# Kernel tuning notes

Hardware: AMD Instinct MI355X
Metric: run time of the kernel (lower is better)

The kernel has to match this reference:

```python
import jax, jax.numpy as jnp
import numpy as np


def setup_inputs() -> dict:
    key = jax.random.key(0)
    ks = jax.random.split(key, 5)
    B, C, H, W = 8, 64, 64, 64
    Ci = 32  # inter_channels = in_channels // 2
    s = 1.0 / np.sqrt(C)
    return {
        "x": jax.random.normal(ks[0], (B, C, H, W), jnp.float32),
        "Wg": jax.random.normal(ks[1], (Ci, C), jnp.float32) * s,
        "bg": jnp.zeros((Ci,), jnp.float32),
        "Wt": jax.random.normal(ks[2], (Ci, C), jnp.float32) * s,
        "bt": jnp.zeros((Ci,), jnp.float32),
        "Wp": jax.random.normal(ks[3], (Ci, C), jnp.float32) * s,
        "bp": jnp.zeros((Ci,), jnp.float32),
        "Ww": jax.random.normal(ks[4], (C, Ci), jnp.float32) * (1.0 / np.sqrt(Ci)),
        "bw": jnp.zeros((C,), jnp.float32),
    }


def _proj(x, Wc, bc):
    # 1x1 conv: (B,C,H,W) -> (B,O,H,W), then flatten spatial -> (B,O,N)
    b, c, h, w = x.shape
    y = jnp.einsum("oc,bchw->bohw", Wc, x) + bc[None, :, None, None]
    return y.reshape(b, Wc.shape[0], h * w)


def reference(x, Wg, bg, Wt, bt, Wp, bp, Ww, bw):
    b, c, h, w = x.shape
    g_x = _proj(x, Wg, bg).transpose(0, 2, 1)      # (B, N, Ci)
    theta_x = _proj(x, Wt, bt).transpose(0, 2, 1)  # (B, N, Ci)
    phi_x = _proj(x, Wp, bp)                        # (B, Ci, N)
    f = jnp.einsum("bnd,bdm->bnm", theta_x, phi_x)  # (B, N, N)
    f_div_C = jax.nn.softmax(f, axis=-1)
    y = jnp.einsum("bnm,bmd->bnd", f_div_C, g_x)    # (B, N, Ci)
    y = y.transpose(0, 2, 1).reshape(b, Wg.shape[0], h, w)
    W_y = jnp.einsum("od,bdhw->bohw", Ww, y) + bw[None, :, None, None]
    return W_y + x
```

## Files before the change

kernel.cpp:

```cpp
#include <hip/hip_runtime.h>
#include <hip/hip_bf16.h>
#include <cstdint>
#include <cstddef>

#define B_ 8
#define C_ 64
#define CI 32
#define N_ 4096

typedef __attribute__((ext_vector_type(8))) short bf16x8;
typedef __attribute__((ext_vector_type(4))) float f32x4;

__device__ __forceinline__ ushort f2bf(float x) {
  union { float f; uint32_t u; } v; v.f = x;
  uint32_t r = v.u + 0x7FFFu + ((v.u >> 16) & 1u);
  return (ushort)(r >> 16);
}

__device__ __forceinline__ uint32_t cvt_pk_bf16(float lo, float hi) {
  uint32_t r;
  asm("v_cvt_pk_bf16_f32 %0, %1, %2" : "=v"(r) : "v"(lo), "v"(hi));
  return r;
}

__global__ __launch_bounds__(256) void proj_kernel(
    const float* __restrict__ x,
    const float* __restrict__ Wg, const float* __restrict__ bg,
    const float* __restrict__ Wt, const float* __restrict__ bt,
    const float* __restrict__ Wp, const float* __restrict__ bp,
    ushort* __restrict__ theta_t, ushort* __restrict__ phi_t,
    ushort* __restrict__ gmat)
{
  const int z = blockIdx.z;
  const float* W; const float* bias;
  if (z == 0)      { W = Wt; bias = bt; }
  else if (z == 1) { W = Wp; bias = bp; }
  else             { W = Wg; bias = bg; }

  const int b = blockIdx.y;
  const int n = blockIdx.x * 256 + threadIdx.x;
  const float* xb = x + ((size_t)b * C_) * N_ + n;

  float acc[CI];
  #pragma unroll
  for (int d = 0; d < CI; ++d) acc[d] = bias[d];

  #pragma unroll
  for (int cc = 0; cc < C_; cc += 8) {
    float xv[8];
    #pragma unroll
    for (int j = 0; j < 8; ++j) xv[j] = xb[(size_t)(cc + j) * N_];
    #pragma unroll
    for (int j = 0; j < 8; ++j)
      #pragma unroll
      for (int d = 0; d < CI; ++d)
        acc[d] = fmaf(W[d * C_ + cc + j], xv[j], acc[d]);
  }

  if (z == 2) {
    #pragma unroll
    for (int d = 0; d < CI; ++d)
      gmat[((size_t)(b * CI) + d) * N_ + n] = f2bf(acc[d]);
  } else {
    const float scale = (z == 0) ? 1.44269504088896340736f : 1.0f;
    uint32_t w[CI / 2];
    #pragma unroll
    for (int k = 0; k < CI / 2; ++k)
      w[k] = (uint32_t)f2bf(acc[2 * k] * scale) |
             ((uint32_t)f2bf(acc[2 * k + 1] * scale) << 16);
    ushort* base = (z == 0) ? theta_t : phi_t;
    uint4* dst = (uint4*)(base + ((size_t)(b * N_) + n) * CI);
    #pragma unroll
    for (int k = 0; k < CI / 8; ++k)
      dst[k] = make_uint4(w[4 * k], w[4 * k + 1], w[4 * k + 2], w[4 * k + 3]);
  }
}

__global__ __launch_bounds__(512, 4) void attn_kernel(
    const ushort* __restrict__ theta_t,
    const ushort* __restrict__ phi_t,
    const ushort* __restrict__ gmat,
    float* __restrict__ yT)
{
  __shared__ ushort Kt[2][64 * 32];
  __shared__ ushort Vt[2][32 * 64];
  __shared__ ushort Pt[8][16 * 64];
  __shared__ float scratch[4][64][12];

  const int tid = threadIdx.x;
  const int lane = tid & 63;
  const int wave = tid >> 6;
  const int qg = wave & 3;
  const int mh = wave >> 2;
  const int bid = blockIdx.x;
  const int b = bid & 7;
  const int n0 = (bid >> 3) * 64;
  const int nw = n0 + qg * 16;
  const int g4 = lane >> 4;
  const int c16 = lane & 15;
  const int sw = (c16 & 7) << 4;

  const bf16x8 qfrag =
      *(const bf16x8*)(theta_t + ((size_t)(b * N_ + nw + c16)) * CI + g4 * 8);

  bf16x8 onesA;
  {
    const short ov = (c16 == 0) ? (short)0x3F80 : (short)0;
    #pragma unroll
    for (int j = 0; j < 8; ++j) onesA[j] = ov;
  }

  f32x4 acc0 = {0.f, 0.f, 0.f, 0.f};
  f32x4 acc1 = {0.f, 0.f, 0.f, 0.f};
  f32x4 acc2 = {0.f, 0.f, 0.f, 0.f};
  float m_run = -INFINITY;

  const char* kf_base = (const char*)Kt[mh] + ((c16 * 64 + g4 * 16) ^ sw);
  char* pw[4];
  #pragma unroll
  for (int mt = 0; mt < 4; ++mt)
    pw[mt] = (char*)Pt[wave] + ((c16 * 128 + mt * 32 + g4 * 8) ^ sw);
  const char* pr[2]; const char* vr[2];
  #pragma unroll
  for (int ks = 0; ks < 2; ++ks) {
    pr[ks] = (const char*)Pt[wave] + ((c16 * 128 + ks * 64 + g4 * 16) ^ sw);
    vr[ks] = (const char*)Vt[mh] + ((c16 * 128 + ks * 64 + g4 * 16) ^ sw);
  }

  const int khalf = tid >> 8;
  const int krem = tid & 255;
  const int km = krem >> 2, kpart = krem & 3;
  const int vd = krem >> 3, vp8 = krem & 7;
  const ushort* kp = phi_t + ((size_t)(b * N_ + khalf * 2048 + km)) * CI + kpart * 8;
  const ushort* vsp = gmat + ((size_t)(b * CI + vd)) * N_ + khalf * 2048 + vp8 * 8;
  char* kdst = (char*)Kt[khalf] + ((km * 64 + kpart * 16) ^ ((km & 7) << 4));
  char* vdst = (char*)Vt[khalf] + ((vd * 128 + vp8 * 16) ^ ((vd & 7) << 4));

  uint4 kreg = *(const uint4*)kp;  kp += 64 * CI;
  uint4 vreg = *(const uint4*)vsp; vsp += 64;
  *(uint4*)kdst = kreg;
  *(uint4*)vdst = vreg;
  __syncthreads();

  const int NT = 2048 / 64;
  for (int t = 0; t < NT; ++t) {
    const bool more = (t + 1 < NT);
    if (more) {
      kreg = *(const uint4*)kp;  kp += 64 * CI;
      vreg = *(const uint4*)vsp; vsp += 64;
    }

    f32x4 f[4];
    __builtin_amdgcn_s_setprio(1);
    #pragma unroll
    for (int mt = 0; mt < 4; ++mt) {
      const bf16x8 kf = *(const bf16x8*)(kf_base + mt * 1024);
      f[mt] = __builtin_amdgcn_mfma_f32_16x16x32_bf16(
          kf, qfrag, (f32x4){0.f, 0.f, 0.f, 0.f}, 0, 0, 0);
    }
    __builtin_amdgcn_s_setprio(0);

    float pm = fmaxf(
        fmaxf(fmaxf(fmaxf(f[0][0], f[0][1]), fmaxf(f[0][2], f[0][3])),
              fmaxf(fmaxf(f[1][0], f[1][1]), fmaxf(f[1][2], f[1][3]))),
        fmaxf(fmaxf(fmaxf(f[2][0], f[2][1]), fmaxf(f[2][2], f[2][3])),
              fmaxf(fmaxf(f[3][0], f[3][1]), fmaxf(f[3][2], f[3][3]))));
    pm = fmaxf(pm, __shfl_xor(pm, 16));
    pm = fmaxf(pm, __shfl_xor(pm, 32));

    if (__any(pm > m_run + 8.f)) {
      const float mnew = fmaxf(m_run, pm);
      const float sc = __builtin_amdgcn_exp2f(m_run - mnew);
      m_run = mnew;
      acc0 *= sc; acc1 *= sc; acc2 *= sc;
    }

    #pragma unroll
    for (int mt = 0; mt < 4; ++mt) {
      const float p0 = __builtin_amdgcn_exp2f(f[mt][0] - m_run);
      const float p1 = __builtin_amdgcn_exp2f(f[mt][1] - m_run);
      const float p2 = __builtin_amdgcn_exp2f(f[mt][2] - m_run);
      const float p3 = __builtin_amdgcn_exp2f(f[mt][3] - m_run);
      uint2 wv;
      wv.x = cvt_pk_bf16(p0, p1);
      wv.y = cvt_pk_bf16(p2, p3);
      *(uint2*)pw[mt] = wv;
    }
    asm volatile("s_waitcnt lgkmcnt(0)" ::: "memory");

    __builtin_amdgcn_s_setprio(1);
    #pragma unroll
    for (int ks = 0; ks < 2; ++ks) {
      const bf16x8 pfrag = *(const bf16x8*)pr[ks];
      const bf16x8 vf0 = *(const bf16x8*)vr[ks];
      const bf16x8 vf1 = *(const bf16x8*)(vr[ks] + 2048);
      acc0 = __builtin_amdgcn_mfma_f32_16x16x32_bf16(vf0, pfrag, acc0, 0, 0, 0);
      acc1 = __builtin_amdgcn_mfma_f32_16x16x32_bf16(vf1, pfrag, acc1, 0, 0, 0);
      acc2 = __builtin_amdgcn_mfma_f32_16x16x32_bf16(onesA, pfrag, acc2, 0, 0, 0);
    }
    __builtin_amdgcn_s_setprio(0);

    __syncthreads();
    if (more) { *(uint4*)kdst = kreg; *(uint4*)vdst = vreg; }
    __syncthreads();
  }

  const float l_own = __shfl(acc2[0], c16, 64);

  if (mh == 1) {
    float* s = scratch[qg][lane];
    s[0] = m_run; s[1] = l_own;
    #pragma unroll
    for (int r = 0; r < 4; ++r) { s[2 + r] = acc0[r]; s[6 + r] = acc1[r]; }
  }
  __syncthreads();
  if (mh == 0) {
    const float* s = scratch[qg][lane];
    const float mb = s[0], lb = s[1];
    const float mM = fmaxf(m_run, mb);
    const float ea = __builtin_amdgcn_exp2f(m_run - mM);
    const float eb = __builtin_amdgcn_exp2f(mb - mM);
    const float inv = 1.0f / (l_own * ea + lb * eb);
    const float fa = ea * inv, fb = eb * inv;
    #pragma unroll
    for (int r = 0; r < 4; ++r) {
      yT[((size_t)(b * CI + g4 * 4 + r)) * N_ + nw + c16] =
          acc0[r] * fa + s[2 + r] * fb;
      yT[((size_t)(b * CI + 16 + g4 * 4 + r)) * N_ + nw + c16] =
          acc1[r] * fa + s[6 + r] * fb;
    }
  }
}

__global__ __launch_bounds__(256) void outproj_kernel(
    const float* __restrict__ yT, const float* __restrict__ Ww,
    const float* __restrict__ bw, const float* __restrict__ x,
    float* __restrict__ out)
{
  const int b = blockIdx.y;
  const int c0 = blockIdx.z * 16;
  const int n = blockIdx.x * 256 + threadIdx.x;
  float acc[16];
  #pragma unroll
  for (int i = 0; i < 16; ++i) acc[i] = bw[c0 + i];
  #pragma unroll
  for (int dd = 0; dd < CI; dd += 8) {
    float yv[8];
    #pragma unroll
    for (int j = 0; j < 8; ++j)
      yv[j] = yT[((size_t)(b * CI + dd + j)) * N_ + n];
    #pragma unroll
    for (int j = 0; j < 8; ++j)
      #pragma unroll
      for (int i = 0; i < 16; ++i)
        acc[i] = fmaf(Ww[(c0 + i) * CI + dd + j], yv[j], acc[i]);
  }
  #pragma unroll
  for (int i = 0; i < 16; ++i) {
    const size_t idx = ((size_t)(b * C_ + c0 + i)) * N_ + n;
    out[idx] = acc[i] + x[idx];
  }
}

extern "C" void kernel_launch(void* const* d_in, const int* in_sizes, int n_in,
                              void* d_out, int out_size, void* d_ws, size_t ws_size,
                              hipStream_t stream) {
  const float* x  = (const float*)d_in[0];
  const float* Wg = (const float*)d_in[1];
  const float* bg = (const float*)d_in[2];
  const float* Wt = (const float*)d_in[3];
  const float* bt = (const float*)d_in[4];
  const float* Wp = (const float*)d_in[5];
  const float* bp = (const float*)d_in[6];
  const float* Ww = (const float*)d_in[7];
  const float* bw = (const float*)d_in[8];
  float* out = (float*)d_out;

  char* ws = (char*)d_ws;
  ushort* theta_t = (ushort*)(ws);
  ushort* phi_t   = (ushort*)(ws + (size_t)2 * 1024 * 1024);
  ushort* gmat    = (ushort*)(ws + (size_t)4 * 1024 * 1024);
  float*  yT      = (float*)(ws + (size_t)6 * 1024 * 1024);

  proj_kernel<<<dim3(N_ / 256, B_, 3), 256, 0, stream>>>(
      x, Wg, bg, Wt, bt, Wp, bp, theta_t, phi_t, gmat);
  attn_kernel<<<dim3(N_ / 64 * B_), 512, 0, stream>>>(
      theta_t, phi_t, gmat, yT);
  outproj_kernel<<<dim3(N_ / 256, B_, 4), 256, 0, stream>>>(
      yT, Ww, bw, x, out);
}
```

Before: 74.30 us.

## Fuse output projection into attention and restructure waves over key splits

Attention blocks now use 4 waves, each processing all 64 queries over a quarter of the keys. K and V fragments are loaded directly from global memory into registers instead of staged in LDS, removing per-tile block barriers. The row sum is accumulated on the VALU instead of via an extra MFMA, and the four key-split partial states are merged through LDS. The 1x1 output projection and residual are fused into the attention kernel, eliminating the yT intermediate and one launch. The projection kernel splits output channels across waves to cut register pressure. The risk is extra global/L2 traffic from per-wave K/V loads and a serialised merge stage.

```diff
diff --git a/kernel.cpp b/kernel.cpp
--- a/kernel.cpp
+++ b/kernel.cpp
@@ -7,17 +7,18 @@
 #define C_ 64
 #define CI 32
 #define N_ 4096
+#define LOG2E 1.44269504088896340736f
 
 typedef __attribute__((ext_vector_type(8))) short bf16x8;
 typedef __attribute__((ext_vector_type(4))) float f32x4;
 
-__device__ __forceinline__ ushort f2bf(float x) {
+static __device__ __forceinline__ ushort f2bf(float x) {
   union { float f; uint32_t u; } v; v.f = x;
   uint32_t r = v.u + 0x7FFFu + ((v.u >> 16) & 1u);
   return (ushort)(r >> 16);
 }
 
-__device__ __forceinline__ uint32_t cvt_pk_bf16(float lo, float hi) {
+static __device__ __forceinline__ uint32_t cvt_pk_bf16(float lo, float hi) {
   uint32_t r;
   asm("v_cvt_pk_bf16_f32 %0, %1, %2" : "=v"(r) : "v"(lo), "v"(hi));
   return r;
@@ -38,227 +39,247 @@
   else             { W = Wg; bias = bg; }
 
   const int b = blockIdx.y;
-  const int n = blockIdx.x * 256 + threadIdx.x;
+  const int t = threadIdx.x;
+  const int n = blockIdx.x * 64 + (t & 63);
+  const int dq = t >> 6;
   const float* xb = x + ((size_t)b * C_) * N_ + n;
-
-  float acc[CI];
-  #pragma unroll
-  for (int d = 0; d < CI; ++d) acc[d] = bias[d];
-
-  #pragma unroll
-  for (int cc = 0; cc < C_; cc += 8) {
-    float xv[8];
-    #pragma unroll
-    for (int j = 0; j < 8; ++j) xv[j] = xb[(size_t)(cc + j) * N_];
-    #pragma unroll
-    for (int j = 0; j < 8; ++j)
-      #pragma unroll
-      for (int d = 0; d < CI; ++d)
-        acc[d] = fmaf(W[d * C_ + cc + j], xv[j], acc[d]);
+  const float* Wr = W + dq * 8 * C_;
+
+  float acc[8];
+  #pragma unroll
+  for (int i = 0; i < 8; ++i) acc[i] = bias[dq * 8 + i];
+
+  #pragma unroll 8
+  for (int c = 0; c < C_; ++c) {
+    const float xv = xb[(size_t)c * N_];
+    #pragma unroll
+    for (int i = 0; i < 8; ++i)
+      acc[i] = fmaf(Wr[i * C_ + c], xv, acc[i]);
   }
 
   if (z == 2) {
     #pragma unroll
-    for (int d = 0; d < CI; ++d)
-      gmat[((size_t)(b * CI) + d) * N_ + n] = f2bf(acc[d]);
+    for (int i = 0; i < 8; ++i)
+      gmat[((size_t)(b * CI) + dq * 8 + i) * N_ + n] = f2bf(acc[i]);
   } else {
-    const float scale = (z == 0) ? 1.44269504088896340736f : 1.0f;
-    uint32_t w[CI / 2];
-    #pragma unroll
-    for (int k = 0; k < CI / 2; ++k)
+    const float scale = (z == 0) ? LOG2E : 1.0f;
+    uint32_t w[4];
+    #pragma unroll
+    for (int k = 0; k < 4; ++k)
       w[k] = (uint32_t)f2bf(acc[2 * k] * scale) |
              ((uint32_t)f2bf(acc[2 * k + 1] * scale) << 16);
     ushort* base = (z == 0) ? theta_t : phi_t;
-    uint4* dst = (uint4*)(base + ((size_t)(b * N_) + n) * CI);
-    #pragma unroll
-    for (int k = 0; k < CI / 8; ++k)
-      dst[k] = make_uint4(w[4 * k], w[4 * k + 1], w[4 * k + 2], w[4 * k + 3]);
-  }
-}
-
-__global__ __launch_bounds__(512, 4) void attn_kernel(
+    *(uint4*)(base + ((size_t)(b * N_) + n) * CI + dq * 8) =
+        make_uint4(w[0], w[1], w[2], w[3]);
+  }
+}
+
+__global__ __launch_bounds__(256, 2) void attn_kernel(
     const ushort* __restrict__ theta_t,
     const ushort* __restrict__ phi_t,
     const ushort* __restrict__ gmat,
-    float* __restrict__ yT)
+    const float* __restrict__ Ww, const float* __restrict__ bw,
+    const float* __restrict__ x, float* __restrict__ out)
 {
-  __shared__ ushort Kt[2][64 * 32];
-  __shared__ ushort Vt[2][32 * 64];
-  __shared__ ushort Pt[8][16 * 64];
-  __shared__ float scratch[4][64][12];
+  __shared__ float scratch[2][64][40];
+  __shared__ ushort Pt[4][2][16 * 64];
+  __shared__ float WwL[C_ * CI];
 
   const int tid = threadIdx.x;
   const int lane = tid & 63;
-  const int wave = tid >> 6;
-  const int qg = wave & 3;
-  const int mh = wave >> 2;
+  const int mh = tid >> 6;
   const int bid = blockIdx.x;
   const int b = bid & 7;
   const int n0 = (bid >> 3) * 64;
-  const int nw = n0 + qg * 16;
   const int g4 = lane >> 4;
   const int c16 = lane & 15;
   const int sw = (c16 & 7) << 4;
 
-  const bf16x8 qfrag =
-      *(const bf16x8*)(theta_t + ((size_t)(b * N_ + nw + c16)) * CI + g4 * 8);
-
-  bf16x8 onesA;
-  {
-    const short ov = (c16 == 0) ? (short)0x3F80 : (short)0;
-    #pragma unroll
-    for (int j = 0; j < 8; ++j) onesA[j] = ov;
-  }
-
-  f32x4 acc0 = {0.f, 0.f, 0.f, 0.f};
-  f32x4 acc1 = {0.f, 0.f, 0.f, 0.f};
-  f32x4 acc2 = {0.f, 0.f, 0.f, 0.f};
-  float m_run = -INFINITY;
-
-  const char* kf_base = (const char*)Kt[mh] + ((c16 * 64 + g4 * 16) ^ sw);
-  char* pw[4];
+  #pragma unroll
+  for (int i = 0; i < 8; ++i) WwL[tid + i * 256] = Ww[tid + i * 256];
+
+  bf16x8 qfrag[4];
+  #pragma unroll
+  for (int s = 0; s < 4; ++s)
+    qfrag[s] = *(const bf16x8*)(theta_t +
+        ((size_t)(b * N_ + n0 + s * 16 + c16)) * CI + g4 * 8);
+
+  f32x4 acc[4][2];
+  #pragma unroll
+  for (int s = 0; s < 4; ++s)
+    #pragma unroll
+    for (int dk = 0; dk < 2; ++dk) acc[s][dk] = (f32x4){0.f, 0.f, 0.f, 0.f};
+  float m_run[4] = {0.f, 0.f, 0.f, 0.f};
+  float l_lane[4] = {0.f, 0.f, 0.f, 0.f};
+
+  const int mq0 = mh * 1024;
+  const ushort* kbase = phi_t + ((size_t)(b * N_ + mq0 + c16)) * CI + g4 * 8;
+  const ushort* vb0 = gmat + ((size_t)(b * CI + c16)) * N_ + mq0 + g4 * 8;
+  const ushort* vb1 = vb0 + (size_t)16 * N_;
+
+  char* pw[2][4]; const char* prd[2][2];
+  #pragma unroll
+  for (int pb = 0; pb < 2; ++pb) {
+    #pragma unroll
+    for (int mt = 0; mt < 4; ++mt)
+      pw[pb][mt] = (char*)Pt[mh][pb] + ((c16 * 128 + mt * 32 + g4 * 8) ^ sw);
+    #pragma unroll
+    for (int ks = 0; ks < 2; ++ks)
+      prd[pb][ks] = (const char*)Pt[mh][pb] + ((c16 * 128 + ks * 64 + g4 * 16) ^ sw);
+  }
+
+  bf16x8 kf[4];
   #pragma unroll
   for (int mt = 0; mt < 4; ++mt)
-    pw[mt] = (char*)Pt[wave] + ((c16 * 128 + mt * 32 + g4 * 8) ^ sw);
-  const char* pr[2]; const char* vr[2];
-  #pragma unroll
-  for (int ks = 0; ks < 2; ++ks) {
-    pr[ks] = (const char*)Pt[wave] + ((c16 * 128 + ks * 64 + g4 * 16) ^ sw);
-    vr[ks] = (const char*)Vt[mh] + ((c16 * 128 + ks * 64 + g4 * 16) ^ sw);
-  }
-
-  const int khalf = tid >> 8;
-  const int krem = tid & 255;
-  const int km = krem >> 2, kpart = krem & 3;
-  const int vd = krem >> 3, vp8 = krem & 7;
-  const ushort* kp = phi_t + ((size_t)(b * N_ + khalf * 2048 + km)) * CI + kpart * 8;
-  const ushort* vsp = gmat + ((size_t)(b * CI + vd)) * N_ + khalf * 2048 + vp8 * 8;
-  char* kdst = (char*)Kt[khalf] + ((km * 64 + kpart * 16) ^ ((km & 7) << 4));
-  char* vdst = (char*)Vt[khalf] + ((vd * 128 + vp8 * 16) ^ ((vd & 7) << 4));
-
-  uint4 kreg = *(const uint4*)kp;  kp += 64 * CI;
-  uint4 vreg = *(const uint4*)vsp; vsp += 64;
-  *(uint4*)kdst = kreg;
-  *(uint4*)vdst = vreg;
-  __syncthreads();
-
-  const int NT = 2048 / 64;
+    kf[mt] = *(const bf16x8*)(kbase + (size_t)(mt * 16) * CI);
+
+  const int NT = 16;
   for (int t = 0; t < NT; ++t) {
-    const bool more = (t + 1 < NT);
-    if (more) {
-      kreg = *(const uint4*)kp;  kp += 64 * CI;
-      vreg = *(const uint4*)vsp; vsp += 64;
-    }
-
-    f32x4 f[4];
-    __builtin_amdgcn_s_setprio(1);
-    #pragma unroll
-    for (int mt = 0; mt < 4; ++mt) {
-      const bf16x8 kf = *(const bf16x8*)(kf_base + mt * 1024);
-      f[mt] = __builtin_amdgcn_mfma_f32_16x16x32_bf16(
-          kf, qfrag, (f32x4){0.f, 0.f, 0.f, 0.f}, 0, 0, 0);
-    }
-    __builtin_amdgcn_s_setprio(0);
-
-    float pm = fmaxf(
-        fmaxf(fmaxf(fmaxf(f[0][0], f[0][1]), fmaxf(f[0][2], f[0][3])),
-              fmaxf(fmaxf(f[1][0], f[1][1]), fmaxf(f[1][2], f[1][3]))),
-        fmaxf(fmaxf(fmaxf(f[2][0], f[2][1]), fmaxf(f[2][2], f[2][3])),
-              fmaxf(fmaxf(f[3][0], f[3][1]), fmaxf(f[3][2], f[3][3]))));
-    pm = fmaxf(pm, __shfl_xor(pm, 16));
-    pm = fmaxf(pm, __shfl_xor(pm, 32));
-
-    if (__any(pm > m_run + 8.f)) {
-      const float mnew = fmaxf(m_run, pm);
-      const float sc = __builtin_amdgcn_exp2f(m_run - mnew);
-      m_run = mnew;
-      acc0 *= sc; acc1 *= sc; acc2 *= sc;
-    }
-
-    #pragma unroll
-    for (int mt = 0; mt < 4; ++mt) {
-      const float p0 = __builtin_amdgcn_exp2f(f[mt][0] - m_run);
-      const float p1 = __builtin_amdgcn_exp2f(f[mt][1] - m_run);
-      const float p2 = __builtin_amdgcn_exp2f(f[mt][2] - m_run);
-      const float p3 = __builtin_amdgcn_exp2f(f[mt][3] - m_run);
-      uint2 wv;
-      wv.x = cvt_pk_bf16(p0, p1);
-      wv.y = cvt_pk_bf16(p2, p3);
-      *(uint2*)pw[mt] = wv;
-    }
-    asm volatile("s_waitcnt lgkmcnt(0)" ::: "memory");
-
-    __builtin_amdgcn_s_setprio(1);
+    bf16x8 vf0[2], vf1[2];
     #pragma unroll
     for (int ks = 0; ks < 2; ++ks) {
-      const bf16x8 pfrag = *(const bf16x8*)pr[ks];
-      const bf16x8 vf0 = *(const bf16x8*)vr[ks];
-      const bf16x8 vf1 = *(const bf16x8*)(vr[ks] + 2048);
-      acc0 = __builtin_amdgcn_mfma_f32_16x16x32_bf16(vf0, pfrag, acc0, 0, 0, 0);
-      acc1 = __builtin_amdgcn_mfma_f32_16x16x32_bf16(vf1, pfrag, acc1, 0, 0, 0);
-      acc2 = __builtin_amdgcn_mfma_f32_16x16x32_bf16(onesA, pfrag, acc2, 0, 0, 0);
-    }
-    __builtin_amdgcn_s_setprio(0);
-
-    __syncthreads();
-    if (more) { *(uint4*)kdst = kreg; *(uint4*)vdst = vreg; }
-    __syncthreads();
-  }
-
-  const float l_own = __shfl(acc2[0], c16, 64);
-
-  if (mh == 1) {
-    float* s = scratch[qg][lane];
-    s[0] = m_run; s[1] = l_own;
-    #pragma unroll
-    for (int r = 0; r < 4; ++r) { s[2 + r] = acc0[r]; s[6 + r] = acc1[r]; }
-  }
-  __syncthreads();
+      vf0[ks] = *(const bf16x8*)(vb0 + t * 64 + ks * 32);
+      vf1[ks] = *(const bf16x8*)(vb1 + t * 64 + ks * 32);
+    }
+    const int tn = (t + 1 < NT) ? t + 1 : t;
+    bf16x8 kfn[4];
+    #pragma unroll
+    for (int mt = 0; mt < 4; ++mt)
+      kfn[mt] = *(const bf16x8*)(kbase + (size_t)(tn * 64 + mt * 16) * CI);
+
+    #pragma unroll
+    for (int s = 0; s < 4; ++s) {
+      const int pb = s & 1;
+      f32x4 f[4];
+      __builtin_amdgcn_s_setprio(1);
+      #pragma unroll
+      for (int mt = 0; mt < 4; ++mt)
+        f[mt] = __builtin_amdgcn_mfma_f32_16x16x32_bf16(
+            kf[mt], qfrag[s], (f32x4){0.f, 0.f, 0.f, 0.f}, 0, 0, 0);
+      __builtin_amdgcn_s_setprio(0);
+
+      float pm = -1e30f;
+      float pv[4][4];
+      #pragma unroll
+      for (int mt = 0; mt < 4; ++mt) {
+        #pragma unroll
+        for (int r = 0; r < 4; ++r) {
+          const float fv = f[mt][r];
+          pm = fmaxf(pm, fv);
+          pv[mt][r] = __builtin_amdgcn_exp2f(fv - m_run[s]);
+        }
+        l_lane[s] += (pv[mt][0] + pv[mt][1]) + (pv[mt][2] + pv[mt][3]);
+      }
+      #pragma unroll
+      for (int mt = 0; mt < 4; ++mt) {
+        uint2 wv;
+        wv.x = cvt_pk_bf16(pv[mt][0], pv[mt][1]);
+        wv.y = cvt_pk_bf16(pv[mt][2], pv[mt][3]);
+        *(uint2*)pw[pb][mt] = wv;
+      }
+      asm volatile("s_waitcnt lgkmcnt(0)" ::: "memory");
+      __builtin_amdgcn_sched_barrier(0);
+
+      __builtin_amdgcn_s_setprio(1);
+      #pragma unroll
+      for (int ks = 0; ks < 2; ++ks) {
+        const bf16x8 pfrag = *(const bf16x8*)prd[pb][ks];
+        acc[s][0] = __builtin_amdgcn_mfma_f32_16x16x32_bf16(
+            vf0[ks], pfrag, acc[s][0], 0, 0, 0);
+        acc[s][1] = __builtin_amdgcn_mfma_f32_16x16x32_bf16(
+            vf1[ks], pfrag, acc[s][1], 0, 0, 0);
+      }
+      __builtin_amdgcn_s_setprio(0);
+
+      if (__any(pm > m_run[s] + 8.f)) {
+        float pmr = fmaxf(pm, __shfl_xor(pm, 16));
+        pmr = fmaxf(pmr, __shfl_xor(pmr, 32));
+        const float mnew = fmaxf(m_run[s], pmr);
+        const float sc = __builtin_amdgcn_exp2f(m_run[s] - mnew);
+        m_run[s] = mnew;
+        acc[s][0] *= sc; acc[s][1] *= sc; l_lane[s] *= sc;
+      }
+    }
+    #pragma unroll
+    for (int mt = 0; mt < 4; ++mt) kf[mt] = kfn[mt];
+  }
+
+  #pragma unroll
+  for (int s = 0; s < 4; ++s) {
+    l_lane[s] += __shfl_xor(l_lane[s], 16);
+    l_lane[s] += __shfl_xor(l_lane[s], 32);
+  }
+
+  auto store_state = [&](float* sp) {
+    #pragma unroll
+    for (int s = 0; s < 4; ++s) {
+      sp[s * 10 + 0] = m_run[s]; sp[s * 10 + 1] = l_lane[s];
+      #pragma unroll
+      for (int r = 0; r < 4; ++r) {
+        sp[s * 10 + 2 + r] = acc[s][0][r];
+        sp[s * 10 + 6 + r] = acc[s][1][r];
+      }
+    }
+  };
+  auto merge_state = [&](const float* sp) {
+    #pragma unroll
+    for (int s = 0; s < 4; ++s) {
+      const float mb = sp[s * 10 + 0], lb = sp[s * 10 + 1];
+      const float mM = fmaxf(m_run[s], mb);
+      const float ea = __builtin_amdgcn_exp2f(m_run[s] - mM);
+      const float eb = __builtin_amdgcn_exp2f(mb - mM);
+      #pragma unroll
+      for (int r = 0; r < 4; ++r) {
+        acc[s][0][r] = acc[s][0][r] * ea + sp[s * 10 + 2 + r] * eb;
+        acc[s][1][r] = acc[s][1][r] * ea + sp[s * 10 + 6 + r] * eb;
+      }
+      l_lane[s] = l_lane[s] * ea + lb * eb;
+      m_run[s] = mM;
+    }
+  };
+
+  if (mh == 1) store_state(scratch[0][lane]);
+  if (mh == 3) store_state(scratch[1][lane]);
+  __syncthreads();
+  if (mh == 0) merge_state(scratch[0][lane]);
+  if (mh == 2) merge_state(scratch[1][lane]);
+  __syncthreads();
+  if (mh == 2) store_state(scratch[0][lane]);
+  __syncthreads();
+  if (mh == 0) merge_state(scratch[0][lane]);
+  __syncthreads();
+
+  float* yl = &scratch[0][0][0];
   if (mh == 0) {
-    const float* s = scratch[qg][lane];
-    const float mb = s[0], lb = s[1];
-    const float mM = fmaxf(m_run, mb);
-    const float ea = __builtin_amdgcn_exp2f(m_run - mM);
-    const float eb = __builtin_amdgcn_exp2f(mb - mM);
-    const float inv = 1.0f / (l_own * ea + lb * eb);
-    const float fa = ea * inv, fb = eb * inv;
-    #pragma unroll
-    for (int r = 0; r < 4; ++r) {
-      yT[((size_t)(b * CI + g4 * 4 + r)) * N_ + nw + c16] =
-          acc0[r] * fa + s[2 + r] * fb;
-      yT[((size_t)(b * CI + 16 + g4 * 4 + r)) * N_ + nw + c16] =
-          acc1[r] * fa + s[6 + r] * fb;
-    }
-  }
-}
-
-__global__ __launch_bounds__(256) void outproj_kernel(
-    const float* __restrict__ yT, const float* __restrict__ Ww,
-    const float* __restrict__ bw, const float* __restrict__ x,
-    float* __restrict__ out)
-{
-  const int b = blockIdx.y;
-  const int c0 = blockIdx.z * 16;
-  const int n = blockIdx.x * 256 + threadIdx.x;
-  float acc[16];
-  #pragma unroll
-  for (int i = 0; i < 16; ++i) acc[i] = bw[c0 + i];
-  #pragma unroll
-  for (int dd = 0; dd < CI; dd += 8) {
-    float yv[8];
-    #pragma unroll
-    for (int j = 0; j < 8; ++j)
-      yv[j] = yT[((size_t)(b * CI + dd + j)) * N_ + n];
-    #pragma unroll
-    for (int j = 0; j < 8; ++j)
-      #pragma unroll
-      for (int i = 0; i < 16; ++i)
-        acc[i] = fmaf(Ww[(c0 + i) * CI + dd + j], yv[j], acc[i]);
+    #pragma unroll
+    for (int s = 0; s < 4; ++s) {
+      const float inv = 1.0f / l_lane[s];
+      const int q = s * 16 + c16;
+      #pragma unroll
+      for (int r = 0; r < 4; ++r) {
+        yl[(g4 * 4 + r) * 66 + q]      = acc[s][0][r] * inv;
+        yl[(16 + g4 * 4 + r) * 66 + q] = acc[s][1][r] * inv;
+      }
+    }
+  }
+  __syncthreads();
+
+  const int nl = tid & 63;
+  const int cg = tid >> 6;
+  float oacc[16];
+  #pragma unroll
+  for (int i = 0; i < 16; ++i) oacc[i] = bw[cg * 16 + i];
+  #pragma unroll
+  for (int d = 0; d < CI; ++d) {
+    const float yv = yl[d * 66 + nl];
+    #pragma unroll
+    for (int i = 0; i < 16; ++i)
+      oacc[i] = fmaf(WwL[(cg * 16 + i) * CI + d], yv, oacc[i]);
   }
   #pragma unroll
   for (int i = 0; i < 16; ++i) {
-    const size_t idx = ((size_t)(b * C_ + c0 + i)) * N_ + n;
-    out[idx] = acc[i] + x[idx];
+    const size_t idx = ((size_t)(b * C_ + cg * 16 + i)) * N_ + n0 + nl;
+    out[idx] = oacc[i] + x[idx];
   }
 }
 
@@ -280,12 +301,9 @@
   ushort* theta_t = (ushort*)(ws);
   ushort* phi_t   = (ushort*)(ws + (size_t)2 * 1024 * 1024);
   ushort* gmat    = (ushort*)(ws + (size_t)4 * 1024 * 1024);
-  float*  yT      = (float*)(ws + (size_t)6 * 1024 * 1024);
-
-  proj_kernel<<<dim3(N_ / 256, B_, 3), 256, 0, stream>>>(
+
+  proj_kernel<<<dim3(N_ / 64, B_, 3), 256, 0, stream>>>(
       x, Wg, bg, Wt, bt, Wp, bp, theta_t, phi_t, gmat);
-  attn_kernel<<<dim3(N_ / 64 * B_), 512, 0, stream>>>(
-      theta_t, phi_t, gmat, yT);
-  outproj_kernel<<<dim3(N_ / 256, B_, 4), 256, 0, stream>>>(
-      yT, Ww, bw, x, out);
-}
+  attn_kernel<<<dim3((N_ / 64) * B_), 256, 0, stream>>>(
+      theta_t, phi_t, gmat, Ww, bw, x, out);
+}
```

Result: no change. 74.00 us (-0.4%).
